# Kernel tuning notes

Measured on AMD Instinct MI355X. Metric: run time of the kernel, lower is better.

Reference implementation:

```python
import jax, jax.numpy as jnp
import numpy as np

NA = 50000   # nodes of type 'a'
NB = 50000   # nodes of type 'b'
E = 800000   # edges per cross relation
D = 256      # input feature dim == hidden_dim (SAGEConv lazy in-dim)
H = 256      # hidden_dim
EMB = 128    # embedding_dim
L = 2        # num_layer
# relation order in stacked weights: 0=(a,to,b), 1=(b,to,a), 2=(a,self_loop,a), 3=(b,self_loop,b)


def setup_inputs() -> dict:
    key = jax.random.key(0)
    ks = jax.random.split(key, 8)
    x_a = jax.random.normal(ks[0], (NA, D), jnp.float32)
    x_b = jax.random.normal(ks[1], (NB, D), jnp.float32)
    edge_ab = jax.random.randint(ks[2], (2, E), 0, NA, dtype=jnp.int32)  # row0: src in a, row1: dst in b
    edge_ba = jax.random.randint(ks[3], (2, E), 0, NB, dtype=jnp.int32)  # row0: src in b, row1: dst in a
    s = 1.0 / np.sqrt(H)
    Wl = jax.random.normal(ks[4], (L, 4, H, H), jnp.float32) * s  # lin_l weight (on aggregated neighbors)
    bl = jnp.zeros((L, 4, H), jnp.float32)                         # lin_l bias
    Wr = jax.random.normal(ks[5], (L, 4, H, H), jnp.float32) * s  # lin_r weight (root/self), no bias
    lin_W = jax.random.normal(ks[6], (H, EMB), jnp.float32) * s
    lin_b = jnp.zeros((EMB,), jnp.float32)
    return dict(x_a=x_a, x_b=x_b, edge_ab=edge_ab, edge_ba=edge_ba,
                Wl=Wl, bl=bl, Wr=Wr, lin_W=lin_W, lin_b=lin_b)


def _sage(x_src, x_dst, src, dst, n_dst, Wl, bl, Wr):
    # SAGEConv: mean-aggregate neighbor features, then lin_l(agg) + lin_r(x_dst)
    agg = jax.ops.segment_sum(x_src[src], dst, num_segments=n_dst)           # [n_dst, H]
    cnt = jax.ops.segment_sum(jnp.ones(src.shape, x_src.dtype), dst, num_segments=n_dst)
    mean = agg / jnp.maximum(cnt, 1.0)[:, None]                               # isolated dst -> 0
    return mean @ Wl + bl + x_dst @ Wr


def _sage_self(x, Wl, bl, Wr):
    # self-loop relation: each node has exactly one neighbor (itself), mean == x
    return x @ Wl + bl + x @ Wr


def reference(x_a, x_b, edge_ab, edge_ba, Wl, bl, Wr, lin_W, lin_b):
    xa, xb = x_a, x_b
    for l in range(L):
        new_a = (_sage(xb, xa, edge_ba[0], edge_ba[1], xa.shape[0], Wl[l, 1], bl[l, 1], Wr[l, 1])
                 + _sage_self(xa, Wl[l, 2], bl[l, 2], Wr[l, 2]))
        new_b = (_sage(xa, xb, edge_ab[0], edge_ab[1], xb.shape[0], Wl[l, 0], bl[l, 0], Wr[l, 0])
                 + _sage_self(xb, Wl[l, 3], bl[l, 3], Wr[l, 3]))
        xa, xb = jax.nn.relu(new_a), jax.nn.relu(new_b)
    return xa @ lin_W + lin_b, xb @ lin_W + lin_b
```

## Files before the change

### kernel.cpp

```cpp
#include <hip/hip_runtime.h>
#include <hip/hip_bf16.h>

#define NNA 50000
#define NNB 50000
#define NE  800000
#define HD  256
#define EMBD 128

typedef __attribute__((ext_vector_type(4))) int            i32x4;
typedef __attribute__((ext_vector_type(4))) float          f32x4;
typedef __attribute__((ext_vector_type(8))) short          bf16x8;
typedef __attribute__((ext_vector_type(4))) unsigned short u16x4;
typedef __attribute__((ext_vector_type(8))) unsigned short u16x8;

static __device__ __forceinline__ float bf2f(unsigned short u) {
  union { unsigned int i; float f; } v; v.i = ((unsigned int)u) << 16; return v.f;
}
static __device__ __forceinline__ unsigned short f2bf(float f) {
  __hip_bfloat16 h = __float2bfloat16(f);
  return *reinterpret_cast<unsigned short*>(&h);
}


__global__ void k_prep_wcat(const float* __restrict__ Wl, const float* __restrict__ Wr,
                            unsigned short* __restrict__ WcatT) {
  int id = blockIdx.x * 256 + threadIdx.x;
  if (id >= 2 * 2 * 512 * 256) return;
  int n = id & 255;
  int k = (id >> 8) & 511;
  int t = (id >> 17) & 1;
  int l = id >> 18;
  int rn = (t == 0) ? 1 : 0;
  int rs = (t == 0) ? 2 : 3;
  float v;
  if (k < HD) {
    v = Wl[((l * 4 + rn) * HD + k) * HD + n];
  } else {
    int kk = k - HD;
    v = Wr[((l * 4 + rn) * HD + kk) * HD + n]
      + Wl[((l * 4 + rs) * HD + kk) * HD + n]
      + Wr[((l * 4 + rs) * HD + kk) * HD + n];
  }
  WcatT[((l * 2 + t) * HD + n) * 512 + k] = f2bf(v);
}

__global__ void k_prep_bias(const float* __restrict__ bl, float* __restrict__ bias) {
  int id = blockIdx.x * 256 + threadIdx.x;
  if (id >= 2 * 2 * 256) return;
  int n = id & 255; int t = (id >> 8) & 1; int l = id >> 9;
  int rn = (t == 0) ? 1 : 0;
  int rs = (t == 0) ? 2 : 3;
  bias[id] = bl[(l * 4 + rn) * HD + n] + bl[(l * 4 + rs) * HD + n];
}

__global__ void k_prep_lin(const float* __restrict__ linW, unsigned short* __restrict__ linWT) {
  int id = blockIdx.x * 256 + threadIdx.x;
  if (id >= EMBD * HD) return;
  int k = id & 255; int n = id >> 8;
  linWT[n * HD + k] = f2bf(linW[k * EMBD + n]);
}

__global__ void k_f32_to_bf16(const float* __restrict__ in, unsigned short* __restrict__ out, int n4) {
  int i = blockIdx.x * blockDim.x + threadIdx.x;
  int stride = gridDim.x * blockDim.x;
  for (; i < n4; i += stride) {
    f32x4 v = reinterpret_cast<const f32x4*>(in)[i];
    u16x4 o;
    o[0] = f2bf(v[0]); o[1] = f2bf(v[1]); o[2] = f2bf(v[2]); o[3] = f2bf(v[3]);
    reinterpret_cast<u16x4*>(out)[i] = o;
  }
}


__global__ void k_fill_slots(const int* __restrict__ edges, int* __restrict__ cnt,
                             int* __restrict__ slots, int nE) {
  int e = blockIdx.x * 256 + threadIdx.x;
  if (e >= nE) return;
  int src = edges[e];
  int dst = edges[nE + e];
  int pos = atomicAdd(&cnt[dst], 1);
  if (pos < 64) slots[dst * 64 + pos] = src;
}

__global__ __launch_bounds__(256)
void k_aggregate(const unsigned short* __restrict__ xa,
                 const unsigned short* __restrict__ xb,
                 const int* __restrict__ slots_a, const int* __restrict__ cnt_a,
                 const int* __restrict__ slots_b, const int* __restrict__ cnt_b,
                 unsigned short* __restrict__ mean_a, unsigned short* __restrict__ mean_b) {
  int w = blockIdx.x * 4 + (threadIdx.x >> 6);
  int lane = threadIdx.x & 63;
  const unsigned short* xsrc;
  const int* sl;
  int deg;
  unsigned short* outp;
  if (w < NNA) {
    xsrc = xb; sl = slots_a + (size_t)w * 64; deg = cnt_a[w];
    outp = mean_a + (size_t)w * HD;
  } else {
    int v = w - NNA;
    xsrc = xa; sl = slots_b + (size_t)v * 64; deg = cnt_b[v];
    outp = mean_b + (size_t)v * HD;
  }
  int m = deg < 64 ? deg : 64;
  int s_all = sl[lane];
  const int half = lane >> 5;
  const int l31 = lane & 31;

  float acc[8];
#pragma unroll
  for (int k = 0; k < 8; ++k) acc[k] = 0.f;

  int j = 0;
  for (; j + 8 <= m; j += 8) {
    int sj[4];
#pragma unroll
    for (int i = 0; i < 4; ++i) sj[i] = __shfl(s_all, j + 2 * i + half);
    u16x8 v[4];
#pragma unroll
    for (int i = 0; i < 4; ++i)
      v[i] = *reinterpret_cast<const u16x8*>(xsrc + (size_t)sj[i] * HD + l31 * 8);
#pragma unroll
    for (int i = 0; i < 4; ++i)
#pragma unroll
      for (int k = 0; k < 8; ++k) acc[k] += bf2f(v[i][k]);
  }
  for (; j + 2 <= m; j += 2) {
    int sj = __shfl(s_all, j + half);
    u16x8 v = *reinterpret_cast<const u16x8*>(xsrc + (size_t)sj * HD + l31 * 8);
#pragma unroll
    for (int k = 0; k < 8; ++k) acc[k] += bf2f(v[k]);
  }
  if (j < m && half == 0) {
    int sj = __shfl(s_all, j);
    u16x8 v = *reinterpret_cast<const u16x8*>(xsrc + (size_t)sj * HD + l31 * 8);
#pragma unroll
    for (int k = 0; k < 8; ++k) acc[k] += bf2f(v[k]);
  }

#pragma unroll
  for (int k = 0; k < 8; ++k) acc[k] += __shfl_xor(acc[k], 32);

  float inv = deg > 0 ? 1.0f / (float)deg : 0.0f;
  if (half == 0) {
    u16x8 o;
#pragma unroll
    for (int k = 0; k < 8; ++k) o[k] = f2bf(acc[k] * inv);
    *reinterpret_cast<u16x8*>(outp + l31 * 8) = o;
  }
}

template <bool RELU, bool OUTF32>
__global__ __launch_bounds__(256)
void k_gemm(const unsigned short* __restrict__ Alo,
            const unsigned short* __restrict__ Ahi,
            const unsigned short* __restrict__ BT,
            const float* __restrict__ bias,
            void* __restrict__ Cout,
            int M, int N, int Ktot, int Klo,
            long long sA, long long sB, long long sBias, long long sCbytes) {
  const int z = blockIdx.z;
  Alo += (long long)z * sA;
  Ahi += (long long)z * sA;
  BT += (long long)z * sB;
  bias += (long long)z * sBias;
  Cout = (void*)((char*)Cout + (long long)z * sCbytes);

  __shared__ char smem[32768];
  const int t = threadIdx.x;
  const int bm = blockIdx.x, bn = blockIdx.y;
  const int lane = t & 63, wid = t >> 6;
  const int wm = wid >> 1, wn = wid & 1;
  const int l15 = lane & 15, l4 = lane >> 4;
  const int rowA0 = t >> 3;
  const int seg = t & 7;

  f32x4 acc[4][4];
#pragma unroll
  for (int i = 0; i < 4; ++i)
#pragma unroll
    for (int j = 0; j < 4; ++j) acc[i][j] = (f32x4){0.f, 0.f, 0.f, 0.f};

  const int nks = Ktot >> 6;
  for (int ks = 0; ks < nks; ++ks) {
    const int kglob = ks << 6;
    const unsigned short* Asrc = (kglob < Klo) ? Alo : Ahi;
    const int kbase = (kglob < Klo) ? kglob : (kglob - Klo);
    i32x4 ra[4], rb[4];
#pragma unroll
    for (int p = 0; p < 4; ++p) {
      int row = rowA0 + p * 32;
      int rg = bm * 128 + row;
      if (rg < M)
        ra[p] = *reinterpret_cast<const i32x4*>(Asrc + (size_t)rg * HD + kbase + seg * 8);
      else
        ra[p] = (i32x4){0, 0, 0, 0};
      int ng = bn * 128 + row;
      rb[p] = *reinterpret_cast<const i32x4*>(BT + (size_t)ng * Ktot + kglob + seg * 8);
    }
    __syncthreads();
#pragma unroll
    for (int p = 0; p < 4; ++p) {
      int row = rowA0 + p * 32;
      int off = row * 128 + ((seg * 16) ^ ((row & 7) << 4));
      *reinterpret_cast<i32x4*>(smem + off) = ra[p];
      *reinterpret_cast<i32x4*>(smem + 16384 + off) = rb[p];
    }
    __syncthreads();
#pragma unroll
    for (int kk = 0; kk < 2; ++kk) {
      bf16x8 af[4], bfr[4];
#pragma unroll
      for (int f = 0; f < 4; ++f) {
        int r = wm * 64 + f * 16 + l15;
        af[f] = *reinterpret_cast<const bf16x8*>(
            smem + r * 128 + ((kk * 64 + l4 * 16) ^ ((r & 7) << 4)));
        int n = wn * 64 + f * 16 + l15;
        bfr[f] = *reinterpret_cast<const bf16x8*>(
            smem + 16384 + n * 128 + ((kk * 64 + l4 * 16) ^ ((n & 7) << 4)));
      }
#pragma unroll
      for (int fm = 0; fm < 4; ++fm)
#pragma unroll
        for (int fn = 0; fn < 4; ++fn)
          acc[fm][fn] = __builtin_amdgcn_mfma_f32_16x16x32_bf16(af[fm], bfr[fn], acc[fm][fn], 0, 0, 0);
    }
  }

#pragma unroll
  for (int fm = 0; fm < 4; ++fm) {
    int row0 = bm * 128 + wm * 64 + fm * 16 + l4 * 4;
#pragma unroll
    for (int fn = 0; fn < 4; ++fn) {
      int col = bn * 128 + wn * 64 + fn * 16 + l15;
      float bv = bias[col];
      f32x4 d = acc[fm][fn];
#pragma unroll
      for (int r = 0; r < 4; ++r) {
        int rg = row0 + r;
        if (rg < M) {
          float v = d[r] + bv;
          if (RELU) v = v > 0.f ? v : 0.f;
          if (OUTF32)
            reinterpret_cast<float*>(Cout)[(size_t)rg * N + col] = v;
          else
            reinterpret_cast<unsigned short*>(Cout)[(size_t)rg * N + col] = f2bf(v);
        }
      }
    }
  }
}


extern "C" void kernel_launch(void* const* d_in, const int* in_sizes, int n_in,
                              void* d_out, int out_size, void* d_ws, size_t ws_size,
                              hipStream_t stream) {
  const float* x_a  = (const float*)d_in[0];
  const float* x_b  = (const float*)d_in[1];
  const int*   e_ab = (const int*)d_in[2];
  const int*   e_ba = (const int*)d_in[3];
  const float* Wl   = (const float*)d_in[4];
  const float* bl   = (const float*)d_in[5];
  const float* Wr   = (const float*)d_in[6];
  const float* linW = (const float*)d_in[7];
  const float* linb = (const float*)d_in[8];
  float* out = (float*)d_out;

  char* ws = (char*)d_ws;
  size_t off = 0;
  auto alloc = [&](size_t bytes) {
    char* p = ws + off;
    off += (bytes + 255) & ~(size_t)255;
    return p;
  };
  unsigned short* x0   = (unsigned short*)alloc((size_t)2 * NNA * HD * 2);
  unsigned short* x1   = (unsigned short*)alloc((size_t)2 * NNA * HD * 2);
  unsigned short* mean = (unsigned short*)alloc((size_t)2 * NNA * HD * 2);
  int* slots_a = (int*)alloc((size_t)NNA * 64 * 4);
  int* slots_b = (int*)alloc((size_t)NNB * 64 * 4);
  int* cnt_a   = (int*)alloc((size_t)NNA * 4);
  int* cnt_b   = (int*)alloc((size_t)NNB * 4);
  unsigned short* wcatT  = (unsigned short*)alloc((size_t)2 * 2 * 256 * 512 * 2);
  float*          biasv  = (float*)alloc((size_t)2 * 2 * 256 * 4);
  unsigned short* linWT  = (unsigned short*)alloc((size_t)EMBD * HD * 2);
  (void)ws_size; (void)in_sizes; (void)n_in; (void)out_size;

  hipMemsetAsync(cnt_a, 0, (size_t)NNA * 4, stream);
  hipMemsetAsync(cnt_b, 0, (size_t)NNB * 4, stream);

  k_prep_wcat<<<2048, 256, 0, stream>>>(Wl, Wr, wcatT);
  k_prep_bias<<<4, 256, 0, stream>>>(bl, biasv);
  k_prep_lin<<<128, 256, 0, stream>>>(linW, linWT);

  k_f32_to_bf16<<<2048, 256, 0, stream>>>(x_a, x0, NNA * HD / 4);
  k_f32_to_bf16<<<2048, 256, 0, stream>>>(x_b, x0 + (size_t)NNA * HD, NNB * HD / 4);

  k_fill_slots<<<(NE + 255) / 256, 256, 0, stream>>>(e_ba, cnt_a, slots_a, NE);
  k_fill_slots<<<(NE + 255) / 256, 256, 0, stream>>>(e_ab, cnt_b, slots_b, NE);

  unsigned short* xcur = x0;
  unsigned short* xnxt = x1;

  for (int l = 0; l < 2; ++l) {
    k_aggregate<<<(NNA + NNB) / 4, 256, 0, stream>>>(
        xcur, xcur + (size_t)NNA * HD, slots_a, cnt_a, slots_b, cnt_b,
        mean, mean + (size_t)NNA * HD);
    dim3 g((NNA + 127) / 128, 2, 2);
    k_gemm<true, false><<<g, 256, 0, stream>>>(
        mean, xcur, wcatT + (size_t)l * 2 * 256 * 512, biasv + l * 2 * 256, xnxt,
        NNA, 256, 512, 256,
        (long long)NNA * HD, 256 * 512, 256, (long long)NNA * HD * 2);
    unsigned short* tmp = xcur; xcur = xnxt; xnxt = tmp;
  }

  dim3 gf((NNA + 127) / 128, 1, 2);
  k_gemm<false, true><<<gf, 256, 0, stream>>>(
      xcur, xcur, linWT, linb, out,
      NNA, EMBD, 256, 256,
      (long long)NNA * HD, 0, 0, (long long)NNA * EMBD * 4);
}
```

Baseline: 503.7 us.

## Double-buffer GEMM tiles via direct global-to-LDS loads and merge prep kernels

The GEMM now stages A and B tiles straight into LDS with global_load_lds into two alternating buffers. The next K-step is issued before the current one is computed, so there is one barrier per step instead of two and no register round-trip. Shared memory doubles to 64KB, which may lower occupancy. Separately, the three weight-prep kernels, the two conversion kernels and the two edge-fill kernels are each merged into one launch to cut launch overhead.

```diff
diff --git a/kernel.cpp b/kernel.cpp
--- a/kernel.cpp
+++ b/kernel.cpp
@@ -21,65 +21,81 @@
   return *reinterpret_cast<unsigned short*>(&h);
 }
 
-
-__global__ void k_prep_wcat(const float* __restrict__ Wl, const float* __restrict__ Wr,
-                            unsigned short* __restrict__ WcatT) {
+static __device__ __forceinline__ void gload_lds16(const void* g, void* l) {
+  __builtin_amdgcn_global_load_lds((const __attribute__((address_space(1))) void*)g,
+                                   (__attribute__((address_space(3))) void*)l, 16, 0, 0);
+}
+
+__global__ void k_prep(const float* __restrict__ Wl, const float* __restrict__ Wr,
+                       const float* __restrict__ bl, const float* __restrict__ linW,
+                       unsigned short* __restrict__ WcatT, float* __restrict__ bias,
+                       unsigned short* __restrict__ linWT) {
   int id = blockIdx.x * 256 + threadIdx.x;
-  if (id >= 2 * 2 * 512 * 256) return;
-  int n = id & 255;
-  int k = (id >> 8) & 511;
-  int t = (id >> 17) & 1;
-  int l = id >> 18;
-  int rn = (t == 0) ? 1 : 0;
-  int rs = (t == 0) ? 2 : 3;
-  float v;
-  if (k < HD) {
-    v = Wl[((l * 4 + rn) * HD + k) * HD + n];
-  } else {
-    int kk = k - HD;
-    v = Wr[((l * 4 + rn) * HD + kk) * HD + n]
-      + Wl[((l * 4 + rs) * HD + kk) * HD + n]
-      + Wr[((l * 4 + rs) * HD + kk) * HD + n];
-  }
-  WcatT[((l * 2 + t) * HD + n) * 512 + k] = f2bf(v);
-}
-
-__global__ void k_prep_bias(const float* __restrict__ bl, float* __restrict__ bias) {
-  int id = blockIdx.x * 256 + threadIdx.x;
-  if (id >= 2 * 2 * 256) return;
-  int n = id & 255; int t = (id >> 8) & 1; int l = id >> 9;
-  int rn = (t == 0) ? 1 : 0;
-  int rs = (t == 0) ? 2 : 3;
-  bias[id] = bl[(l * 4 + rn) * HD + n] + bl[(l * 4 + rs) * HD + n];
-}
-
-__global__ void k_prep_lin(const float* __restrict__ linW, unsigned short* __restrict__ linWT) {
-  int id = blockIdx.x * 256 + threadIdx.x;
-  if (id >= EMBD * HD) return;
-  int k = id & 255; int n = id >> 8;
-  linWT[n * HD + k] = f2bf(linW[k * EMBD + n]);
-}
-
-__global__ void k_f32_to_bf16(const float* __restrict__ in, unsigned short* __restrict__ out, int n4) {
+  if (id < 2 * 2 * 512 * 256) {
+    int n = id & 255;
+    int k = (id >> 8) & 511;
+    int t = (id >> 17) & 1;
+    int l = id >> 18;
+    int rn = (t == 0) ? 1 : 0;
+    int rs = (t == 0) ? 2 : 3;
+    float v;
+    if (k < HD) {
+      v = Wl[((l * 4 + rn) * HD + k) * HD + n];
+    } else {
+      int kk = k - HD;
+      v = Wr[((l * 4 + rn) * HD + kk) * HD + n]
+        + Wl[((l * 4 + rs) * HD + kk) * HD + n]
+        + Wr[((l * 4 + rs) * HD + kk) * HD + n];
+    }
+    WcatT[((l * 2 + t) * HD + n) * 512 + k] = f2bf(v);
+    return;
+  }
+  int id1 = id - 2 * 2 * 512 * 256;
+  if (id1 < 2 * 2 * 256) {
+    int n = id1 & 255; int t = (id1 >> 8) & 1; int l = id1 >> 9;
+    int rn = (t == 0) ? 1 : 0;
+    int rs = (t == 0) ? 2 : 3;
+    bias[id1] = bl[(l * 4 + rn) * HD + n] + bl[(l * 4 + rs) * HD + n];
+    return;
+  }
+  int id2 = id1 - 2 * 2 * 256;
+  if (id2 < EMBD * HD) {
+    int k = id2 & 255; int n = id2 >> 8;
+    linWT[n * HD + k] = f2bf(linW[k * EMBD + n]);
+  }
+}
+
+__global__ void k_convert(const float* __restrict__ xa, const float* __restrict__ xb,
+                          unsigned short* __restrict__ out) {
+  const int n4a = NNA * HD / 4;
+  const int n4  = (NNA + NNB) * HD / 4;
   int i = blockIdx.x * blockDim.x + threadIdx.x;
   int stride = gridDim.x * blockDim.x;
   for (; i < n4; i += stride) {
-    f32x4 v = reinterpret_cast<const f32x4*>(in)[i];
+    const float* src = (i < n4a) ? (xa + (size_t)i * 4) : (xb + (size_t)(i - n4a) * 4);
+    f32x4 v = *reinterpret_cast<const f32x4*>(src);
     u16x4 o;
     o[0] = f2bf(v[0]); o[1] = f2bf(v[1]); o[2] = f2bf(v[2]); o[3] = f2bf(v[3]);
     reinterpret_cast<u16x4*>(out)[i] = o;
   }
 }
 
-
-__global__ void k_fill_slots(const int* __restrict__ edges, int* __restrict__ cnt,
-                             int* __restrict__ slots, int nE) {
+__global__ void k_fill(const int* __restrict__ e_ba, const int* __restrict__ e_ab,
+                       int* __restrict__ cnt_a, int* __restrict__ slots_a,
+                       int* __restrict__ cnt_b, int* __restrict__ slots_b) {
   int e = blockIdx.x * 256 + threadIdx.x;
-  if (e >= nE) return;
-  int src = edges[e];
-  int dst = edges[nE + e];
-  int pos = atomicAdd(&cnt[dst], 1);
-  if (pos < 64) slots[dst * 64 + pos] = src;
+  if (e < NE) {
+    int src = e_ba[e];
+    int dst = e_ba[NE + e];
+    int pos = atomicAdd(&cnt_a[dst], 1);
+    if (pos < 64) slots_a[dst * 64 + pos] = src;
+  } else if (e < 2 * NE) {
+    int f = e - NE;
+    int src = e_ab[f];
+    int dst = e_ab[NE + f];
+    int pos = atomicAdd(&cnt_b[dst], 1);
+    if (pos < 64) slots_b[dst * 64 + pos] = src;
+  }
 }
 
 __global__ __launch_bounds__(256)
@@ -166,14 +182,14 @@
   bias += (long long)z * sBias;
   Cout = (void*)((char*)Cout + (long long)z * sCbytes);
 
-  __shared__ char smem[32768];
+  __shared__ char smem[65536];
   const int t = threadIdx.x;
   const int bm = blockIdx.x, bn = blockIdx.y;
   const int lane = t & 63, wid = t >> 6;
   const int wm = wid >> 1, wn = wid & 1;
   const int l15 = lane & 15, l4 = lane >> 4;
-  const int rowA0 = t >> 3;
-  const int seg = t & 7;
+  const int rgrp = lane >> 3;
+  const int boff = (((lane & 7) ^ rgrp) << 4);
 
   f32x4 acc[4][4];
 #pragma unroll
@@ -182,31 +198,33 @@
     for (int j = 0; j < 4; ++j) acc[i][j] = (f32x4){0.f, 0.f, 0.f, 0.f};
 
   const int nks = Ktot >> 6;
-  for (int ks = 0; ks < nks; ++ks) {
+
+  auto stage = [&](int ks, int buf) {
     const int kglob = ks << 6;
     const unsigned short* Asrc = (kglob < Klo) ? Alo : Ahi;
     const int kbase = (kglob < Klo) ? kglob : (kglob - Klo);
-    i32x4 ra[4], rb[4];
-#pragma unroll
-    for (int p = 0; p < 4; ++p) {
-      int row = rowA0 + p * 32;
-      int rg = bm * 128 + row;
-      if (rg < M)
-        ra[p] = *reinterpret_cast<const i32x4*>(Asrc + (size_t)rg * HD + kbase + seg * 8);
-      else
-        ra[p] = (i32x4){0, 0, 0, 0};
-      int ng = bn * 128 + row;
-      rb[p] = *reinterpret_cast<const i32x4*>(BT + (size_t)ng * Ktot + kglob + seg * 8);
+    char* sA_ = smem + buf * 16384;
+    char* sB_ = smem + 32768 + buf * 16384;
+#pragma unroll
+    for (int i = 0; i < 4; ++i) {
+      int rloc = wid * 32 + i * 8;
+      int rA = bm * 128 + rloc + rgrp;
+      if (rA >= M) rA = M - 1;
+      const char* ga = (const char*)(Asrc + (size_t)rA * HD + kbase) + boff;
+      gload_lds16(ga, sA_ + rloc * 128);
+      int rB = bn * 128 + rloc + rgrp;
+      const char* gb = (const char*)(BT + (size_t)rB * Ktot + kglob) + boff;
+      gload_lds16(gb, sB_ + rloc * 128);
     }
-    __syncthreads();
-#pragma unroll
-    for (int p = 0; p < 4; ++p) {
-      int row = rowA0 + p * 32;
-      int off = row * 128 + ((seg * 16) ^ ((row & 7) << 4));
-      *reinterpret_cast<i32x4*>(smem + off) = ra[p];
-      *reinterpret_cast<i32x4*>(smem + 16384 + off) = rb[p];
-    }
-    __syncthreads();
+  };
+
+  stage(0, 0);
+  __syncthreads();
+
+  for (int ks = 0; ks < nks; ++ks) {
+    if (ks + 1 < nks) stage(ks + 1, (ks + 1) & 1);
+    const char* sA_ = smem + (ks & 1) * 16384;
+    const char* sB_ = smem + 32768 + (ks & 1) * 16384;
 #pragma unroll
     for (int kk = 0; kk < 2; ++kk) {
       bf16x8 af[4], bfr[4];
@@ -214,10 +232,10 @@
       for (int f = 0; f < 4; ++f) {
         int r = wm * 64 + f * 16 + l15;
         af[f] = *reinterpret_cast<const bf16x8*>(
-            smem + r * 128 + ((kk * 64 + l4 * 16) ^ ((r & 7) << 4)));
+            sA_ + r * 128 + ((kk * 64 + l4 * 16) ^ ((r & 7) << 4)));
         int n = wn * 64 + f * 16 + l15;
         bfr[f] = *reinterpret_cast<const bf16x8*>(
-            smem + 16384 + n * 128 + ((kk * 64 + l4 * 16) ^ ((n & 7) << 4)));
+            sB_ + n * 128 + ((kk * 64 + l4 * 16) ^ ((n & 7) << 4)));
       }
 #pragma unroll
       for (int fm = 0; fm < 4; ++fm)
@@ -225,6 +243,7 @@
         for (int fn = 0; fn < 4; ++fn)
           acc[fm][fn] = __builtin_amdgcn_mfma_f32_16x16x32_bf16(af[fm], bfr[fn], acc[fm][fn], 0, 0, 0);
     }
+    __syncthreads();
   }
 
 #pragma unroll
@@ -288,15 +307,10 @@
   hipMemsetAsync(cnt_a, 0, (size_t)NNA * 4, stream);
   hipMemsetAsync(cnt_b, 0, (size_t)NNB * 4, stream);
 
-  k_prep_wcat<<<2048, 256, 0, stream>>>(Wl, Wr, wcatT);
-  k_prep_bias<<<4, 256, 0, stream>>>(bl, biasv);
-  k_prep_lin<<<128, 256, 0, stream>>>(linW, linWT);
-
-  k_f32_to_bf16<<<2048, 256, 0, stream>>>(x_a, x0, NNA * HD / 4);
-  k_f32_to_bf16<<<2048, 256, 0, stream>>>(x_b, x0 + (size_t)NNA * HD, NNB * HD / 4);
-
-  k_fill_slots<<<(NE + 255) / 256, 256, 0, stream>>>(e_ba, cnt_a, slots_a, NE);
-  k_fill_slots<<<(NE + 255) / 256, 256, 0, stream>>>(e_ab, cnt_b, slots_b, NE);
+  k_prep<<<(2 * 2 * 512 * 256 + 1024 + 32768 + 255) / 256, 256, 0, stream>>>(
+      Wl, Wr, bl, linW, wcatT, biasv, linWT);
+  k_convert<<<2048, 256, 0, stream>>>(x_a, x_b, x0);
+  k_fill<<<(2 * NE + 255) / 256, 256, 0, stream>>>(e_ba, e_ab, cnt_a, slots_a, cnt_b, slots_b);
 
   unsigned short* xcur = x0;
   unsigned short* xnxt = x1;
```

New measurement: 527.5 us. +4.7%, slower.
